# Optimization experiments

Hardware: AMD Instinct MI355X
Metric: run time of the kernel (lower is better)

The kernel has to match this reference:

```python
import jax, jax.numpy as jnp
import numpy as np

N_NODES = 50000
N_EDGES = 800000
DIMS = [128, 128, 128, 64]  # in, hid1, hid2, out
EPS = 1e-12


def setup_inputs() -> dict:
    key = jax.random.key(0)
    ks = jax.random.split(key, 32)
    inp = {
        "x": jax.random.normal(ks[0], (N_NODES, DIMS[0]), dtype=jnp.float32),
        "edge_src": jax.random.randint(ks[1], (N_EDGES,), 0, N_NODES),
        "edge_dst": jax.random.randint(ks[2], (N_EDGES,), 0, N_NODES),
    }
    k = 3
    for l in range(3):
        din, dout = DIMS[l], DIMS[l + 1]
        s_in = 1.0 / np.sqrt(din)
        inp[f"Wp{l+1}"] = jax.random.uniform(ks[k], (din, din), jnp.float32, -s_in, s_in); k += 1
        inp[f"bp{l+1}"] = jax.random.uniform(ks[k], (din,), jnp.float32, -s_in, s_in); k += 1
        inp[f"Ws{l+1}"] = jax.random.uniform(ks[k], (din, dout), jnp.float32, -s_in, s_in); k += 1
        inp[f"Wn{l+1}"] = jax.random.uniform(ks[k], (din, dout), jnp.float32, -s_in, s_in); k += 1
        inp[f"b{l+1}"] = jnp.zeros((dout,), jnp.float32); k += 1
    return inp


def _sage_pool_layer(x, src, dst, Wp, bp, Ws, Wn, b):
    # per-edge: relu(fc_pool(x_src)); [E, din]
    m = jax.nn.relu(x[src] @ Wp + bp)
    # max-pool over in-neighbors of each dst node; [N, din]
    pooled = jax.ops.segment_max(m, dst, num_segments=x.shape[0])
    deg = jax.ops.segment_sum(jnp.ones((dst.shape[0],), x.dtype), dst,
                              num_segments=x.shape[0])
    pooled = jnp.where(deg[:, None] > 0, pooled, 0.0)  # zero-degree -> 0 (DGL)
    return x @ Ws + pooled @ Wn + b


def _l2norm_relu(h):
    n = jnp.sqrt(jnp.sum(h * h, axis=1, keepdims=True))
    return jax.nn.relu(h / jnp.maximum(n, EPS))


def reference(x, edge_src, edge_dst,
              Wp1, bp1, Ws1, Wn1, b1,
              Wp2, bp2, Ws2, Wn2, b2,
              Wp3, bp3, Ws3, Wn3, b3):
    h = _l2norm_relu(_sage_pool_layer(x, edge_src, edge_dst, Wp1, bp1, Ws1, Wn1, b1))
    h = _l2norm_relu(_sage_pool_layer(h, edge_src, edge_dst, Wp2, bp2, Ws2, Wn2, b2))
    h = _l2norm_relu(_sage_pool_layer(h, edge_src, edge_dst, Wp3, bp3, Ws3, Wn3, b3))
    return h
```

## Files before the change

kernel.cpp:

```cpp
#include <hip/hip_runtime.h>
#include <math.h>

#define N_NODES 50000
#define N_EDGES 800000
#define CAP 64
#define RANGES 8
#define NODES_PER_RANGE 6250
#define GEMMB 782
#define CHUNKS (N_EDGES / 256)
#define CPB 8
#define BPR ((CHUNKS + CPB - 1) / CPB)
#define CSRB (BPR * RANGES)
#define LROW 136

typedef __attribute__((ext_vector_type(8))) short short8;
typedef __attribute__((ext_vector_type(4))) short short4v;
typedef __attribute__((ext_vector_type(4))) float f32x4;

__device__ __forceinline__ unsigned short f2bf(float f) {
    unsigned int u = __float_as_uint(f);
    return (unsigned short)((u + 0x7FFFu + ((u >> 16) & 1u)) >> 16);
}

template <bool F32>
__device__ __forceinline__ short8 loadA(const void* A, int off) {
    short8 r;
    if (F32) {
        const float* p = (const float*)A + off;
        float4 f0 = *(const float4*)p;
        float4 f1 = *(const float4*)(p + 4);
        r[0] = (short)f2bf(f0.x); r[1] = (short)f2bf(f0.y);
        r[2] = (short)f2bf(f0.z); r[3] = (short)f2bf(f0.w);
        r[4] = (short)f2bf(f1.x); r[5] = (short)f2bf(f1.y);
        r[6] = (short)f2bf(f1.z); r[7] = (short)f2bf(f1.w);
    } else {
        r = *(const short8*)((const unsigned short*)A + off);
    }
    return r;
}

struct WDescs { const float* W[9]; int N[9]; };

__global__ __launch_bounds__(256) void prep_kernel(
    WDescs wd, unsigned short* __restrict__ Wpk, int* __restrict__ deg)
{
    const int nthr = gridDim.x * 256;
    const int tid = blockIdx.x * 256 + threadIdx.x;
    for (int id = tid; id < 9 * 16384; id += nthr) {
        int mi = id >> 14;
        int loc = id & 16383;
        int N = wd.N[mi];
        if (loc < 128 * N) {
            int c = loc / (N * 32);
            int n = (loc - c * N * 32) >> 5;
            int k = c * 32 + (loc & 31);
            Wpk[mi * 16384 + loc] = f2bf(wd.W[mi][k * N + n]);
        }
    }
    for (int i = tid; i < N_NODES; i += nthr) deg[i] = 0;
}

__global__ __launch_bounds__(256) void mix_kernel(
    const int* __restrict__ esrc, const int* __restrict__ edst,
    int* __restrict__ deg, unsigned short* __restrict__ csr16,
    const float* __restrict__ x, const unsigned short* __restrict__ Wp1,
    const float* __restrict__ bp1, unsigned short* __restrict__ Y)
{
    if (blockIdx.x >= GEMMB) {
        const int b = blockIdx.x - GEMMB;
        const int range = b & (RANGES - 1);
        const int cbase = (b >> 3) * CPB;
        const int lo = range * NODES_PER_RANGE;
        int d[CPB], s[CPB];
        #pragma unroll
        for (int i = 0; i < CPB; ++i) {
            const int c = cbase + i;
            const int e = c * 256 + threadIdx.x;
            const bool ok = (c < CHUNKS);
            d[i] = ok ? edst[e] : -1;
            s[i] = ok ? esrc[e] : 0;
        }
        #pragma unroll
        for (int i = 0; i < CPB; ++i) {
            if ((unsigned)(d[i] - lo) < (unsigned)NODES_PER_RANGE) {
                int r = atomicAdd(&deg[d[i]], 1);
                if (r < CAP) csr16[(d[i] << 6) + r] = (unsigned short)s[i];
            }
        }
        return;
    }
    const int lane = threadIdx.x & 63;
    const int wv = threadIdx.x >> 6;
    const int cl = lane & 15;
    const int quad = lane >> 4;
    const int rowBase = blockIdx.x * 64 + wv * 16;
    const int ar = min(rowBase + cl, N_NODES - 1);
    const int bLane = cl * 32 + quad * 8;

    f32x4 acc[8];
    #pragma unroll
    for (int t = 0; t < 8; ++t) acc[t] = (f32x4){0.f, 0.f, 0.f, 0.f};

    #pragma unroll
    for (int c = 0; c < 4; ++c) {
        short8 af = loadA<true>(x, ar * 128 + c * 32 + quad * 8);
        const unsigned short* Bc = Wp1 + c * 4096 + bLane;
        #pragma unroll
        for (int t = 0; t < 8; ++t) {
            short8 bf = *(const short8*)(Bc + t * 512);
            acc[t] = __builtin_amdgcn_mfma_f32_16x16x32_bf16(af, bf, acc[t], 0, 0, 0);
        }
    }
    const int row0 = rowBase + quad * 4;
    #pragma unroll
    for (int t = 0; t < 8; ++t) {
        float bc = bp1[t * 16 + cl];
        #pragma unroll
        for (int g = 0; g < 4; ++g) {
            int r = row0 + g;
            if (r < N_NODES)
                Y[r * 128 + t * 16 + cl] = f2bf(fmaxf(acc[t][g] + bc, 0.0f));
        }
    }
}

__global__ __launch_bounds__(256) void pool_max4(
    const unsigned short* __restrict__ y, const int* __restrict__ deg,
    const unsigned short* __restrict__ csr16, unsigned short* __restrict__ pool)
{
    const int wv = threadIdx.x >> 6;
    const int lane = threadIdx.x & 63;
    const int half = lane >> 5;
    const int q = lane & 31;
    const int n = blockIdx.x * 4 + wv;
    const int e0 = n << 6;
    const int e1 = e0 + min(deg[n], CAP);
    const unsigned short* yb = y + 4 * q;

    short4v acc = (short4v){0, 0, 0, 0};
    int e = e0;
    for (; e + 16 <= e1; e += 16) {
        uint2 Ia = *(const uint2*)(csr16 + e + (half << 2));
        uint2 Ib = *(const uint2*)(csr16 + e + 8 + (half << 2));
        int s0 = (int)(Ia.x & 0xFFFF), s1 = (int)(Ia.x >> 16);
        int s2 = (int)(Ia.y & 0xFFFF), s3 = (int)(Ia.y >> 16);
        int s4 = (int)(Ib.x & 0xFFFF), s5 = (int)(Ib.x >> 16);
        int s6 = (int)(Ib.y & 0xFFFF), s7 = (int)(Ib.y >> 16);
        short4v v0 = *(const short4v*)(yb + (s0 << 7));
        short4v v1 = *(const short4v*)(yb + (s1 << 7));
        short4v v2 = *(const short4v*)(yb + (s2 << 7));
        short4v v3 = *(const short4v*)(yb + (s3 << 7));
        short4v v4 = *(const short4v*)(yb + (s4 << 7));
        short4v v5 = *(const short4v*)(yb + (s5 << 7));
        short4v v6 = *(const short4v*)(yb + (s6 << 7));
        short4v v7 = *(const short4v*)(yb + (s7 << 7));
        acc = __builtin_elementwise_max(acc, v0);
        acc = __builtin_elementwise_max(acc, v1);
        acc = __builtin_elementwise_max(acc, v2);
        acc = __builtin_elementwise_max(acc, v3);
        acc = __builtin_elementwise_max(acc, v4);
        acc = __builtin_elementwise_max(acc, v5);
        acc = __builtin_elementwise_max(acc, v6);
        acc = __builtin_elementwise_max(acc, v7);
    }
    for (; e + 8 <= e1; e += 8) {
        uint2 I = *(const uint2*)(csr16 + e + (half << 2));
        int sa = (int)(I.x & 0xFFFF), sb = (int)(I.x >> 16);
        int sc = (int)(I.y & 0xFFFF), sd = (int)(I.y >> 16);
        short4v va = *(const short4v*)(yb + (sa << 7));
        short4v vb = *(const short4v*)(yb + (sb << 7));
        short4v vc = *(const short4v*)(yb + (sc << 7));
        short4v vd = *(const short4v*)(yb + (sd << 7));
        acc = __builtin_elementwise_max(acc, va);
        acc = __builtin_elementwise_max(acc, vb);
        acc = __builtin_elementwise_max(acc, vc);
        acc = __builtin_elementwise_max(acc, vd);
    }
    for (; e < e1; ++e) {
        int s = csr16[e];
        short4v v = *(const short4v*)(yb + (s << 7));
        acc = __builtin_elementwise_max(acc, v);
    }
    int2 ai = *(int2*)&acc;
    int2 bi;
    bi.x = __shfl_xor(ai.x, 32, 64);
    bi.y = __shfl_xor(ai.y, 32, 64);
    short4v other = *(short4v*)&bi;
    acc = __builtin_elementwise_max(acc, other);
    if (half == 0)
        *(short4v*)(pool + n * 128 + 4 * q) = acc;
}

template <bool A0F32, bool LAST>
__global__ __launch_bounds__(256) void dualy_kernel(
    const void* __restrict__ A0,
    const unsigned short* __restrict__ B0, const unsigned short* __restrict__ B1,
    const float* __restrict__ bias,
    const unsigned short* __restrict__ PL,
    unsigned short* __restrict__ outH, float* __restrict__ outF,
    const unsigned short* __restrict__ Bnext, const float* __restrict__ bnext,
    unsigned short* __restrict__ Yout)
{
    constexpr int NT = LAST ? 4 : 8;
    constexpr int N = NT * 16;
    __shared__ unsigned short lds[4][16 * LROW];

    const int lane = threadIdx.x & 63;
    const int wv = threadIdx.x >> 6;
    const int cl = lane & 15;
    const int quad = lane >> 4;
    const int nodeBase = blockIdx.x * 64 + wv * 16;
    unsigned short* plw = &lds[wv][0];

    const int ar = min(nodeBase + cl, N_NODES - 1);
    const int aBase = ar * 128 + quad * 8;
    const int bLane = cl * 32 + quad * 8;

    f32x4 acc[NT];
    #pragma unroll
    for (int t = 0; t < NT; ++t) acc[t] = (f32x4){0.f, 0.f, 0.f, 0.f};

    #pragma unroll
    for (int c = 0; c < 4; ++c) {
        short8 a0 = loadA<A0F32>(A0, aBase + c * 32);
        short8 a1 = *(const short8*)(PL + aBase + c * 32);
        const unsigned short* B0c = B0 + c * (N * 32) + bLane;
        const unsigned short* B1c = B1 + c * (N * 32) + bLane;
        #pragma unroll
        for (int t = 0; t < NT; ++t) {
            short8 bf = *(const short8*)(B0c + t * 512);
            acc[t] = __builtin_amdgcn_mfma_f32_16x16x32_bf16(a0, bf, acc[t], 0, 0, 0);
        }
        #pragma unroll
        for (int t = 0; t < NT; ++t) {
            short8 bf = *(const short8*)(B1c + t * 512);
            acc[t] = __builtin_amdgcn_mfma_f32_16x16x32_bf16(a1, bf, acc[t], 0, 0, 0);
        }
    }

    #pragma unroll
    for (int t = 0; t < NT; ++t) {
        float bc = bias[t * 16 + cl];
        #pragma unroll
        for (int g = 0; g < 4; ++g) acc[t][g] += bc;
    }

    float inv[4];
    #pragma unroll
    for (int g = 0; g < 4; ++g) {
        float s = 0.f;
        #pragma unroll
        for (int t = 0; t < NT; ++t) s += acc[t][g] * acc[t][g];
        s += __shfl_xor(s, 1, 64);
        s += __shfl_xor(s, 2, 64);
        s += __shfl_xor(s, 4, 64);
        s += __shfl_xor(s, 8, 64);
        inv[g] = 1.0f / fmaxf(sqrtf(s), 1e-12f);
    }

    const int row0 = nodeBase + quad * 4;

    if (LAST) {
        #pragma unroll
        for (int t = 0; t < NT; ++t)
            #pragma unroll
            for (int g = 0; g < 4; ++g) {
                int r = row0 + g;
                if (r < N_NODES)
                    outF[r * N + t * 16 + cl] = fmaxf(acc[t][g] * inv[g], 0.0f);
            }
        return;
    }

    #pragma unroll
    for (int t = 0; t < NT; ++t)
        #pragma unroll
        for (int g = 0; g < 4; ++g) {
            int r = row0 + g;
            unsigned short h = f2bf(fmaxf(acc[t][g] * inv[g], 0.0f));
            if (r < N_NODES) outH[r * 128 + t * 16 + cl] = h;
            plw[(quad * 4 + g) * LROW + t * 16 + cl] = h;
        }

    f32x4 ya[8];
    #pragma unroll
    for (int t = 0; t < 8; ++t) ya[t] = (f32x4){0.f, 0.f, 0.f, 0.f};
    #pragma unroll
    for (int c = 0; c < 4; ++c) {
        short8 af = *(const short8*)(plw + cl * LROW + c * 32 + quad * 8);
        const unsigned short* Bc = Bnext + c * 4096 + bLane;
        #pragma unroll
        for (int t = 0; t < 8; ++t) {
            short8 bf = *(const short8*)(Bc + t * 512);
            ya[t] = __builtin_amdgcn_mfma_f32_16x16x32_bf16(af, bf, ya[t], 0, 0, 0);
        }
    }
    #pragma unroll
    for (int t = 0; t < 8; ++t) {
        float bc = bnext[t * 16 + cl];
        #pragma unroll
        for (int g = 0; g < 4; ++g) {
            int r = row0 + g;
            if (r < N_NODES)
                Yout[r * 128 + t * 16 + cl] = f2bf(fmaxf(ya[t][g] + bc, 0.0f));
        }
    }
}

extern "C" void kernel_launch(void* const* d_in, const int* in_sizes, int n_in,
                              void* d_out, int out_size, void* d_ws, size_t ws_size,
                              hipStream_t stream) {
    const float* x    = (const float*)d_in[0];
    const int*   esrc = (const int*)d_in[1];
    const int*   edst = (const int*)d_in[2];
    const float* Wp[3], *bp[3], *Ws[3], *Wn[3], *bb[3];
    for (int l = 0; l < 3; ++l) {
        Wp[l] = (const float*)d_in[3 + 5 * l];
        bp[l] = (const float*)d_in[4 + 5 * l];
        Ws[l] = (const float*)d_in[5 + 5 * l];
        Wn[l] = (const float*)d_in[6 + 5 * l];
        bb[l] = (const float*)d_in[7 + 5 * l];
    }

    const int NF = N_NODES * 128;
    unsigned short* YA  = (unsigned short*)d_ws;
    unsigned short* YB  = YA + NF;
    unsigned short* PL  = YB + NF;
    unsigned short* H1  = PL + NF;
    unsigned short* H2  = H1 + NF;
    unsigned short* Wpk = H2 + NF;
    int* deg = (int*)(Wpk + 9 * 16384);
    unsigned short* csr16 = (unsigned short*)(deg + N_NODES);

    auto WH = [&](int i) { return Wpk + i * 16384; };

    WDescs wd;
    wd.W[0] = Wp[0]; wd.N[0] = 128;
    wd.W[1] = Ws[0]; wd.N[1] = 128;
    wd.W[2] = Wn[0]; wd.N[2] = 128;
    wd.W[3] = Wp[1]; wd.N[3] = 128;
    wd.W[4] = Ws[1]; wd.N[4] = 128;
    wd.W[5] = Wn[1]; wd.N[5] = 128;
    wd.W[6] = Wp[2]; wd.N[6] = 128;
    wd.W[7] = Ws[2]; wd.N[7] = 64;
    wd.W[8] = Wn[2]; wd.N[8] = 64;

    const int poolBlocks = N_NODES / 4;

    prep_kernel<<<576, 256, 0, stream>>>(wd, Wpk, deg);
    mix_kernel<<<GEMMB + CSRB, 256, 0, stream>>>(esrc, edst, deg, csr16,
                                                 x, WH(0), bp[0], YA);
    pool_max4<<<poolBlocks, 256, 0, stream>>>(YA, deg, csr16, PL);
    dualy_kernel<true, false><<<GEMMB, 256, 0, stream>>>(
        x, WH(1), WH(2), bb[0], PL, H1, nullptr, WH(3), bp[1], YB);
    pool_max4<<<poolBlocks, 256, 0, stream>>>(YB, deg, csr16, PL);
    dualy_kernel<false, false><<<GEMMB, 256, 0, stream>>>(
        H1, WH(4), WH(5), bb[1], PL, H2, nullptr, WH(6), bp[2], YA);
    pool_max4<<<poolBlocks, 256, 0, stream>>>(YA, deg, csr16, PL);
    dualy_kernel<false, true><<<GEMMB, 256, 0, stream>>>(
        H2, WH(7), WH(8), bb[2], PL, nullptr, (float*)d_out,
        nullptr, nullptr, nullptr);
}
```

Baseline: 344.3 us.

## Fuse neighbor max-pool gather into the dual GEMM kernel via LDS

Removes the separate pool_max4 kernels and instead gathers each node's pooled neighbor features inside the dual GEMM kernel, staging them in LDS before the MFMA. This eliminates three kernel launches and the global write/read of the pooled buffer. In exchange the gather runs with far fewer blocks, each lane serially walks a node's edge list with per-node divergent trip counts, reducing memory-level parallelism for the latency-bound gather.

```diff
diff --git a/kernel.cpp b/kernel.cpp
--- a/kernel.cpp
+++ b/kernel.cpp
@@ -14,7 +14,6 @@
 #define LROW 136
 
 typedef __attribute__((ext_vector_type(8))) short short8;
-typedef __attribute__((ext_vector_type(4))) short short4v;
 typedef __attribute__((ext_vector_type(4))) float f32x4;
 
 __device__ __forceinline__ unsigned short f2bf(float f) {
@@ -124,79 +123,14 @@
     }
 }
 
-__global__ __launch_bounds__(256) void pool_max4(
-    const unsigned short* __restrict__ y, const int* __restrict__ deg,
-    const unsigned short* __restrict__ csr16, unsigned short* __restrict__ pool)
-{
-    const int wv = threadIdx.x >> 6;
-    const int lane = threadIdx.x & 63;
-    const int half = lane >> 5;
-    const int q = lane & 31;
-    const int n = blockIdx.x * 4 + wv;
-    const int e0 = n << 6;
-    const int e1 = e0 + min(deg[n], CAP);
-    const unsigned short* yb = y + 4 * q;
-
-    short4v acc = (short4v){0, 0, 0, 0};
-    int e = e0;
-    for (; e + 16 <= e1; e += 16) {
-        uint2 Ia = *(const uint2*)(csr16 + e + (half << 2));
-        uint2 Ib = *(const uint2*)(csr16 + e + 8 + (half << 2));
-        int s0 = (int)(Ia.x & 0xFFFF), s1 = (int)(Ia.x >> 16);
-        int s2 = (int)(Ia.y & 0xFFFF), s3 = (int)(Ia.y >> 16);
-        int s4 = (int)(Ib.x & 0xFFFF), s5 = (int)(Ib.x >> 16);
-        int s6 = (int)(Ib.y & 0xFFFF), s7 = (int)(Ib.y >> 16);
-        short4v v0 = *(const short4v*)(yb + (s0 << 7));
-        short4v v1 = *(const short4v*)(yb + (s1 << 7));
-        short4v v2 = *(const short4v*)(yb + (s2 << 7));
-        short4v v3 = *(const short4v*)(yb + (s3 << 7));
-        short4v v4 = *(const short4v*)(yb + (s4 << 7));
-        short4v v5 = *(const short4v*)(yb + (s5 << 7));
-        short4v v6 = *(const short4v*)(yb + (s6 << 7));
-        short4v v7 = *(const short4v*)(yb + (s7 << 7));
-        acc = __builtin_elementwise_max(acc, v0);
-        acc = __builtin_elementwise_max(acc, v1);
-        acc = __builtin_elementwise_max(acc, v2);
-        acc = __builtin_elementwise_max(acc, v3);
-        acc = __builtin_elementwise_max(acc, v4);
-        acc = __builtin_elementwise_max(acc, v5);
-        acc = __builtin_elementwise_max(acc, v6);
-        acc = __builtin_elementwise_max(acc, v7);
-    }
-    for (; e + 8 <= e1; e += 8) {
-        uint2 I = *(const uint2*)(csr16 + e + (half << 2));
-        int sa = (int)(I.x & 0xFFFF), sb = (int)(I.x >> 16);
-        int sc = (int)(I.y & 0xFFFF), sd = (int)(I.y >> 16);
-        short4v va = *(const short4v*)(yb + (sa << 7));
-        short4v vb = *(const short4v*)(yb + (sb << 7));
-        short4v vc = *(const short4v*)(yb + (sc << 7));
-        short4v vd = *(const short4v*)(yb + (sd << 7));
-        acc = __builtin_elementwise_max(acc, va);
-        acc = __builtin_elementwise_max(acc, vb);
-        acc = __builtin_elementwise_max(acc, vc);
-        acc = __builtin_elementwise_max(acc, vd);
-    }
-    for (; e < e1; ++e) {
-        int s = csr16[e];
-        short4v v = *(const short4v*)(yb + (s << 7));
-        acc = __builtin_elementwise_max(acc, v);
-    }
-    int2 ai = *(int2*)&acc;
-    int2 bi;
-    bi.x = __shfl_xor(ai.x, 32, 64);
-    bi.y = __shfl_xor(ai.y, 32, 64);
-    short4v other = *(short4v*)&bi;
-    acc = __builtin_elementwise_max(acc, other);
-    if (half == 0)
-        *(short4v*)(pool + n * 128 + 4 * q) = acc;
-}
-
 template <bool A0F32, bool LAST>
-__global__ __launch_bounds__(256) void dualy_kernel(
+__global__ __launch_bounds__(256) void fused_kernel(
     const void* __restrict__ A0,
+    const unsigned short* __restrict__ Yl,
+    const int* __restrict__ deg,
+    const unsigned short* __restrict__ csr16,
     const unsigned short* __restrict__ B0, const unsigned short* __restrict__ B1,
     const float* __restrict__ bias,
-    const unsigned short* __restrict__ PL,
     unsigned short* __restrict__ outH, float* __restrict__ outF,
     const unsigned short* __restrict__ Bnext, const float* __restrict__ bnext,
     unsigned short* __restrict__ Yout)
@@ -212,8 +146,58 @@
     const int nodeBase = blockIdx.x * 64 + wv * 16;
     unsigned short* plw = &lds[wv][0];
 
+    {
+        const int n16 = lane >> 2;
+        const int g   = lane & 3;
+        const int node = nodeBase + n16;
+        const int myDeg = (node < N_NODES) ? min(deg[node], CAP) : 0;
+        const unsigned short* csrn = csr16 + (node << 6);
+        const unsigned short* yg = Yl + g * 32;
+        short8 p0 = (short8){0,0,0,0,0,0,0,0};
+        short8 p1 = p0, p2 = p0, p3 = p0;
+        for (int k = 0; k < myDeg; k += 4) {
+            uint2 I = *(const uint2*)(csrn + k);
+            const int s0 = (int)(I.x & 0xFFFF), s1 = (int)(I.x >> 16);
+            const int s2 = (int)(I.y & 0xFFFF), s3 = (int)(I.y >> 16);
+            {
+                const short8* r = (const short8*)(yg + (s0 << 7));
+                p0 = __builtin_elementwise_max(p0, r[0]);
+                p1 = __builtin_elementwise_max(p1, r[1]);
+                p2 = __builtin_elementwise_max(p2, r[2]);
+                p3 = __builtin_elementwise_max(p3, r[3]);
+            }
+            if (k + 1 < myDeg) {
+                const short8* r = (const short8*)(yg + (s1 << 7));
+                p0 = __builtin_elementwise_max(p0, r[0]);
+                p1 = __builtin_elementwise_max(p1, r[1]);
+                p2 = __builtin_elementwise_max(p2, r[2]);
+                p3 = __builtin_elementwise_max(p3, r[3]);
+            }
+            if (k + 2 < myDeg) {
+                const short8* r = (const short8*)(yg + (s2 << 7));
+                p0 = __builtin_elementwise_max(p0, r[0]);
+                p1 = __builtin_elementwise_max(p1, r[1]);
+                p2 = __builtin_elementwise_max(p2, r[2]);
+                p3 = __builtin_elementwise_max(p3, r[3]);
+            }
+            if (k + 3 < myDeg) {
+                const short8* r = (const short8*)(yg + (s3 << 7));
+                p0 = __builtin_elementwise_max(p0, r[0]);
+                p1 = __builtin_elementwise_max(p1, r[1]);
+                p2 = __builtin_elementwise_max(p2, r[2]);
+                p3 = __builtin_elementwise_max(p3, r[3]);
+            }
+        }
+        unsigned short* pw = plw + n16 * LROW + g * 32;
+        *(short8*)(pw)      = p0;
+        *(short8*)(pw + 8)  = p1;
+        *(short8*)(pw + 16) = p2;
+        *(short8*)(pw + 24) = p3;
+    }
+
     const int ar = min(nodeBase + cl, N_NODES - 1);
     const int aBase = ar * 128 + quad * 8;
+    const int fBase = cl * LROW + quad * 8;
     const int bLane = cl * 32 + quad * 8;
 
     f32x4 acc[NT];
@@ -223,7 +207,7 @@
     #pragma unroll
     for (int c = 0; c < 4; ++c) {
         short8 a0 = loadA<A0F32>(A0, aBase + c * 32);
-        short8 a1 = *(const short8*)(PL + aBase + c * 32);
+        short8 a1 = *(const short8*)(plw + fBase + c * 32);
         const unsigned short* B0c = B0 + c * (N * 32) + bLane;
         const unsigned short* B1c = B1 + c * (N * 32) + bLane;
         #pragma unroll
@@ -345,19 +329,14 @@
     wd.W[7] = Ws[2]; wd.N[7] = 64;
     wd.W[8] = Wn[2]; wd.N[8] = 64;
 
-    const int poolBlocks = N_NODES / 4;
-
     prep_kernel<<<576, 256, 0, stream>>>(wd, Wpk, deg);
     mix_kernel<<<GEMMB + CSRB, 256, 0, stream>>>(esrc, edst, deg, csr16,
                                                  x, WH(0), bp[0], YA);
-    pool_max4<<<poolBlocks, 256, 0, stream>>>(YA, deg, csr16, PL);
-    dualy_kernel<true, false><<<GEMMB, 256, 0, stream>>>(
-        x, WH(1), WH(2), bb[0], PL, H1, nullptr, WH(3), bp[1], YB);
-    pool_max4<<<poolBlocks, 256, 0, stream>>>(YB, deg, csr16, PL);
-    dualy_kernel<false, false><<<GEMMB, 256, 0, stream>>>(
-        H1, WH(4), WH(5), bb[1], PL, H2, nullptr, WH(6), bp[2], YA);
-    pool_max4<<<poolBlocks, 256, 0, stream>>>(YA, deg, csr16, PL);
-    dualy_kernel<false, true><<<GEMMB, 256, 0, stream>>>(
-        H2, WH(7), WH(8), bb[2], PL, nullptr, (float*)d_out,
+    fused_kernel<true, false><<<GEMMB, 256, 0, stream>>>(
+        x, YA, deg, csr16, WH(1), WH(2), bb[0], H1, nullptr, WH(3), bp[1], YB);
+    fused_kernel<false, false><<<GEMMB, 256, 0, stream>>>(
+        H1, YB, deg, csr16, WH(4), WH(5), bb[1], H2, nullptr, WH(6), bp[2], YA);
+    fused_kernel<false, true><<<GEMMB, 256, 0, stream>>>(
+        H2, YA, deg, csr16, WH(7), WH(8), bb[2], nullptr, (float*)d_out,
         nullptr, nullptr, nullptr);
 }
```

Measured after the change: 336.5 us. 2.3% less time.
